# Performance work log

Measured on AMD Instinct MI355X. Metric: run time of the kernel, lower is better.

## Reference

```python
import jax, jax.numpy as jnp
import numpy as np

N = 50000       # nodes
E = 800000      # edges (avg degree 16)
D_IN = 128
D_H = 128
D_OUT = 64


def setup_inputs() -> dict:
    key = jax.random.key(0)
    ks = jax.random.split(key, 8)
    x = jax.random.normal(ks[0], (N, D_IN), dtype=jnp.float32)
    edge_index = jax.random.randint(ks[1], (2, E), 0, N)
    W1 = jax.random.normal(ks[2], (D_IN, D_H), dtype=jnp.float32) / np.sqrt(D_IN)
    b1 = jnp.zeros((D_H,), dtype=jnp.float32)
    W2 = jax.random.normal(ks[3], (D_H, D_H), dtype=jnp.float32) / np.sqrt(D_H)
    b2 = jnp.zeros((D_H,), dtype=jnp.float32)
    Wfc = jax.random.normal(ks[4], (D_H, D_OUT), dtype=jnp.float32) / np.sqrt(D_H)
    bfc = jnp.zeros((D_OUT,), dtype=jnp.float32)
    return {"x": x, "edge_index": edge_index, "W1": W1, "b1": b1,
            "W2": W2, "b2": b2, "Wfc": Wfc, "bfc": bfc}


def reference(x, edge_index, W1, b1, W2, b2, Wfc, bfc):
    n = x.shape[0]
    # GCNConv (PyG default): add self-loops, symmetric normalization
    loops = jnp.arange(n, dtype=edge_index.dtype)
    src = jnp.concatenate([edge_index[0], loops])
    dst = jnp.concatenate([edge_index[1], loops])
    deg = jax.ops.segment_sum(jnp.ones(src.shape, x.dtype), dst, num_segments=n)
    dinv = jnp.where(deg > 0, jax.lax.rsqrt(deg), jnp.zeros_like(deg))
    norm = dinv[src] * dinv[dst]  # [E + N]

    def gcn_conv(h, W, b):
        hw = h @ W                              # transform first (smaller gather)
        msg = hw[src] * norm[:, None]           # gather + scale
        return jax.ops.segment_sum(msg, dst, num_segments=n) + b  # scatter-add

    h = jax.nn.relu(gcn_conv(x, W1, b1))   # dropout_prob=0 -> identity
    h = jax.nn.relu(gcn_conv(h, W2, b2))
    pooled = jnp.max(h, axis=0)            # custom_global_max_pool over nodes
    return pooled @ Wfc + bfc              # [D_OUT]
```

## Files before the change

### kernel.cpp

```cpp
#include <hip/hip_runtime.h>
#include <cstdint>
#include <cstddef>

typedef unsigned int uint;
typedef unsigned short ushort;

__device__ __forceinline__ ushort f2bf(float f) {
    uint u = __float_as_uint(f);
    u = u + 0x7FFFu + ((u >> 16) & 1u);
    return (ushort)(u >> 16);
}
__device__ __forceinline__ float bf_lo(uint u) { return __uint_as_float((u & 0xFFFFu) << 16); }
__device__ __forceinline__ float bf_hi(uint u) { return __uint_as_float(u & 0xFFFF0000u); }


__global__ __launch_bounds__(256) void k_count(const int* __restrict__ dst,
                                               int* __restrict__ cnt,
                                               int* __restrict__ rank, int E) {
    int e4 = (blockIdx.x * 256 + threadIdx.x) * 4;
    if (e4 + 3 < E) {
        int4 d = *reinterpret_cast<const int4*>(&dst[e4]);
        int4 r;
        r.x = atomicAdd(&cnt[d.x], 1);
        r.y = atomicAdd(&cnt[d.y], 1);
        r.z = atomicAdd(&cnt[d.z], 1);
        r.w = atomicAdd(&cnt[d.w], 1);
        *reinterpret_cast<int4*>(&rank[e4]) = r;
    } else {
        for (int e = e4; e < E; e++)
            rank[e] = atomicAdd(&cnt[dst[e]], 1);
    }
}

__global__ __launch_bounds__(256) void k_block_reduce(const int* __restrict__ cnt,
                                                      int* __restrict__ bsum, int n) {
    __shared__ int sd[256];
    int i = blockIdx.x * 256 + threadIdx.x;
    sd[threadIdx.x] = (i < n) ? cnt[i] : 0;
    __syncthreads();
    for (int s = 128; s > 0; s >>= 1) {
        if (threadIdx.x < s) sd[threadIdx.x] += sd[threadIdx.x + s];
        __syncthreads();
    }
    if (threadIdx.x == 0) bsum[blockIdx.x] = sd[0];
}

__global__ __launch_bounds__(256) void k_scan_write(const int* __restrict__ cnt,
                                                    const int* __restrict__ bsum,
                                                    int* __restrict__ rowptr,
                                                    float* __restrict__ dinv,
                                                    int n, int nb) {
    __shared__ int sd[256];
    int t = threadIdx.x;
    sd[t] = (t < (int)blockIdx.x && t < nb) ? bsum[t] : 0;
    __syncthreads();
    for (int s = 128; s > 0; s >>= 1) {
        if (t < s) sd[t] += sd[t + s];
        __syncthreads();
    }
    int prefix = sd[0];
    __syncthreads();
    int i = blockIdx.x * 256 + t;
    int v = (i < n) ? cnt[i] : 0;
    sd[t] = v;
    __syncthreads();
    for (int off = 1; off < 256; off <<= 1) {
        int add = (t >= off) ? sd[t - off] : 0;
        __syncthreads();
        sd[t] += add;
        __syncthreads();
    }
    int excl = sd[t] - v + prefix;
    if (i < n) {
        rowptr[i] = excl;
        dinv[i] = rsqrtf((float)v + 1.0f);
    }
}

__global__ __launch_bounds__(256) void k_scatter(const int* __restrict__ src,
                                                 const int* __restrict__ dst,
                                                 const int* __restrict__ rowptr,
                                                 const int* __restrict__ rank,
                                                 const float* __restrict__ dinv,
                                                 int2* __restrict__ eSW, int E) {
    int e4 = (blockIdx.x * 256 + threadIdx.x) * 4;
    if (e4 + 3 < E) {
        int4 s = *reinterpret_cast<const int4*>(&src[e4]);
        int4 d = *reinterpret_cast<const int4*>(&dst[e4]);
        int4 r = *reinterpret_cast<const int4*>(&rank[e4]);
        int2 p0, p1, p2, p3;
        p0.x = s.x; p0.y = __float_as_int(dinv[s.x] * dinv[d.x]);
        p1.x = s.y; p1.y = __float_as_int(dinv[s.y] * dinv[d.y]);
        p2.x = s.z; p2.y = __float_as_int(dinv[s.z] * dinv[d.z]);
        p3.x = s.w; p3.y = __float_as_int(dinv[s.w] * dinv[d.w]);
        eSW[rowptr[d.x] + r.x] = p0;
        eSW[rowptr[d.y] + r.y] = p1;
        eSW[rowptr[d.z] + r.z] = p2;
        eSW[rowptr[d.w] + r.w] = p3;
    } else {
        for (int e = e4; e < E; e++) {
            int s = src[e], d = dst[e];
            int2 pp; pp.x = s; pp.y = __float_as_int(dinv[s] * dinv[d]);
            eSW[rowptr[d] + rank[e]] = pp;
        }
    }
}


#define AP 68

__global__ __launch_bounds__(256, 4) void k_gemm128(const float* __restrict__ A,
                                                    const float* __restrict__ Wg,
                                                    ushort* __restrict__ C, int nrows) {
    __shared__ float As[32 * AP];
    __shared__ float Ws[32 * 128];
    const int tid = threadIdx.x;
    const int tc = tid & 15;
    const int tr = tid >> 4;
    const int r0 = blockIdx.x * 64;

    float acc[4][8];
#pragma unroll
    for (int j = 0; j < 4; j++)
#pragma unroll
        for (int c = 0; c < 8; c++) acc[j][c] = 0.0f;

    const float4* A4 = reinterpret_cast<const float4*>(A);
    const float4* Wg4 = reinterpret_cast<const float4*>(Wg);
    float4* Ws4 = reinterpret_cast<float4*>(Ws);

    const int srow = tid >> 3;
    const int sk4 = tid & 7;

    for (int kc = 0; kc < 4; kc++) {
#pragma unroll
        for (int i = 0; i < 4; i++) Ws4[tid + 256 * i] = Wg4[kc * 1024 + tid + 256 * i];
#pragma unroll
        for (int pass = 0; pass < 2; pass++) {
            int rl = srow + pass * 32;
            int rg = r0 + rl;
            if (rg > nrows - 1) rg = nrows - 1;
            float4 av = A4[(size_t)rg * 32 + kc * 8 + sk4];
            int kb = sk4 * 4;
            As[(kb + 0) * AP + rl] = av.x;
            As[(kb + 1) * AP + rl] = av.y;
            As[(kb + 2) * AP + rl] = av.z;
            As[(kb + 3) * AP + rl] = av.w;
        }
        __syncthreads();

#pragma unroll 4
        for (int k = 0; k < 32; k++) {
            const float4 a = *reinterpret_cast<const float4*>(&As[k * AP + tr * 4]);
            const float4 w0 = *reinterpret_cast<const float4*>(&Ws[k * 128 + tc * 8]);
            const float4 w1 = *reinterpret_cast<const float4*>(&Ws[k * 128 + tc * 8 + 4]);
            const float av4[4] = {a.x, a.y, a.z, a.w};
            const float wv[8] = {w0.x, w0.y, w0.z, w0.w, w1.x, w1.y, w1.z, w1.w};
#pragma unroll
            for (int j = 0; j < 4; j++)
#pragma unroll
                for (int c = 0; c < 8; c++)
                    acc[j][c] = fmaf(av4[j], wv[c], acc[j][c]);
        }
        __syncthreads();
    }

#pragma unroll
    for (int j = 0; j < 4; j++) {
        const int r = r0 + tr * 4 + j;
        if (r < nrows) {
            uint4 o;
            o.x = (uint)f2bf(acc[j][0]) | ((uint)f2bf(acc[j][1]) << 16);
            o.y = (uint)f2bf(acc[j][2]) | ((uint)f2bf(acc[j][3]) << 16);
            o.z = (uint)f2bf(acc[j][4]) | ((uint)f2bf(acc[j][5]) << 16);
            o.w = (uint)f2bf(acc[j][6]) | ((uint)f2bf(acc[j][7]) << 16);
            *reinterpret_cast<uint4*>(&C[(size_t)r * 128 + tc * 8]) = o;
        }
    }
}


__global__ __launch_bounds__(256) void k_gather(const ushort* __restrict__ hw,
                                                const float* __restrict__ dinv,
                                                const int* __restrict__ rowptr,
                                                const int* __restrict__ cnt,
                                                const int2* __restrict__ eSW,
                                                const float* __restrict__ bias,
                                                float* __restrict__ outp, int n) {
    int wave = threadIdx.x >> 6;
    int lane = threadIdx.x & 63;
    int half = lane >> 5;
    int sub = lane & 31;
    int node = blockIdx.x * 4 + wave;
    if (node >= n) return;

    float di = dinv[node];
    int start = rowptr[node];
    int deg = cnt[node];

    const uint2* base2 = reinterpret_cast<const uint2*>(hw);
    float a0, a1, a2, a3;
    {
        uint2 u = base2[(size_t)node * 32 + sub];
        float sw = half ? 0.0f : di * di;
        a0 = bf_lo(u.x) * sw; a1 = bf_hi(u.x) * sw;
        a2 = bf_lo(u.y) * sw; a3 = bf_hi(u.y) * sw;
    }

    int j = 0;
    for (; j + 8 <= deg; j += 8) {
        int2 e[4]; uint2 u[4];
#pragma unroll
        for (int t = 0; t < 4; t++) e[t] = eSW[start + j + 2 * t + half];
#pragma unroll
        for (int t = 0; t < 4; t++) u[t] = base2[(size_t)e[t].x * 32 + sub];
#pragma unroll
        for (int t = 0; t < 4; t++) {
            float w = __int_as_float(e[t].y);
            a0 = fmaf(bf_lo(u[t].x), w, a0);
            a1 = fmaf(bf_hi(u[t].x), w, a1);
            a2 = fmaf(bf_lo(u[t].y), w, a2);
            a3 = fmaf(bf_hi(u[t].y), w, a3);
        }
    }
    for (; j < deg; j += 2) {
        int idx = j + half;
        bool ok = idx < deg;
        int2 e = eSW[start + (ok ? idx : deg - 1)];
        float w = ok ? __int_as_float(e.y) : 0.0f;
        uint2 u = base2[(size_t)e.x * 32 + sub];
        a0 = fmaf(bf_lo(u.x), w, a0);
        a1 = fmaf(bf_hi(u.x), w, a1);
        a2 = fmaf(bf_lo(u.y), w, a2);
        a3 = fmaf(bf_hi(u.y), w, a3);
    }

    a0 += __shfl_xor(a0, 32);
    a1 += __shfl_xor(a1, 32);
    a2 += __shfl_xor(a2, 32);
    a3 += __shfl_xor(a3, 32);

    if (half == 0) {
        float4 bb = reinterpret_cast<const float4*>(bias)[sub];
        float4 o;
        o.x = fmaxf(a0 + bb.x, 0.0f);
        o.y = fmaxf(a1 + bb.y, 0.0f);
        o.z = fmaxf(a2 + bb.z, 0.0f);
        o.w = fmaxf(a3 + bb.w, 0.0f);
        reinterpret_cast<float4*>(outp + (size_t)node * 128)[sub] = o;
    }
}


__global__ __launch_bounds__(256) void k_gather_pool(const ushort* __restrict__ hw,
                                                     const float* __restrict__ dinv,
                                                     const int* __restrict__ rowptr,
                                                     const int* __restrict__ cnt,
                                                     const int2* __restrict__ eSW,
                                                     const float* __restrict__ bias,
                                                     int* __restrict__ pooledPart, int n) {
    __shared__ int smax[128];
    int tid = threadIdx.x;
    int wave = tid >> 6;
    int lane = tid & 63;
    int half = lane >> 5;
    int sub = lane & 31;
    if (tid < 128) smax[tid] = 0;
    __syncthreads();

    int node = blockIdx.x * 4 + wave;
    if (node < n) {
        float di = dinv[node];
        int start = rowptr[node];
        int deg = cnt[node];

        const uint2* base2 = reinterpret_cast<const uint2*>(hw);
        float a0, a1, a2, a3;
        {
            uint2 u = base2[(size_t)node * 32 + sub];
            float sw = half ? 0.0f : di * di;
            a0 = bf_lo(u.x) * sw; a1 = bf_hi(u.x) * sw;
            a2 = bf_lo(u.y) * sw; a3 = bf_hi(u.y) * sw;
        }

        int j = 0;
        for (; j + 8 <= deg; j += 8) {
            int2 e[4]; uint2 u[4];
#pragma unroll
            for (int t = 0; t < 4; t++) e[t] = eSW[start + j + 2 * t + half];
#pragma unroll
            for (int t = 0; t < 4; t++) u[t] = base2[(size_t)e[t].x * 32 + sub];
#pragma unroll
            for (int t = 0; t < 4; t++) {
                float w = __int_as_float(e[t].y);
                a0 = fmaf(bf_lo(u[t].x), w, a0);
                a1 = fmaf(bf_hi(u[t].x), w, a1);
                a2 = fmaf(bf_lo(u[t].y), w, a2);
                a3 = fmaf(bf_hi(u[t].y), w, a3);
            }
        }
        for (; j < deg; j += 2) {
            int idx = j + half;
            bool ok = idx < deg;
            int2 e = eSW[start + (ok ? idx : deg - 1)];
            float w = ok ? __int_as_float(e.y) : 0.0f;
            uint2 u = base2[(size_t)e.x * 32 + sub];
            a0 = fmaf(bf_lo(u.x), w, a0);
            a1 = fmaf(bf_hi(u.x), w, a1);
            a2 = fmaf(bf_lo(u.y), w, a2);
            a3 = fmaf(bf_hi(u.y), w, a3);
        }

        a0 += __shfl_xor(a0, 32);
        a1 += __shfl_xor(a1, 32);
        a2 += __shfl_xor(a2, 32);
        a3 += __shfl_xor(a3, 32);

        if (half == 0) {
            float4 bb = reinterpret_cast<const float4*>(bias)[sub];
            a0 = fmaxf(a0 + bb.x, 0.0f);
            a1 = fmaxf(a1 + bb.y, 0.0f);
            a2 = fmaxf(a2 + bb.z, 0.0f);
            a3 = fmaxf(a3 + bb.w, 0.0f);
            atomicMax(&smax[sub * 4 + 0], __float_as_int(a0));
            atomicMax(&smax[sub * 4 + 1], __float_as_int(a1));
            atomicMax(&smax[sub * 4 + 2], __float_as_int(a2));
            atomicMax(&smax[sub * 4 + 3], __float_as_int(a3));
        }
    }
    __syncthreads();
    if (tid < 128) pooledPart[(size_t)blockIdx.x * 128 + tid] = smax[tid];
}


__global__ __launch_bounds__(256) void k_pool2fc(const int* __restrict__ pooledPart,
                                                 int* __restrict__ pooledBits,
                                                 int* __restrict__ ticket,
                                                 const float* __restrict__ Wfc,
                                                 const float* __restrict__ bfc,
                                                 float* __restrict__ out, int nPart) {
    __shared__ int smax[128];
    __shared__ int isLast;
    int tid = threadIdx.x;
    int c = tid & 127;
    int rh = tid >> 7;
    if (tid < 128) smax[tid] = 0;
    __syncthreads();
    int m = 0;
    for (int p = blockIdx.x * 2 + rh; p < nPart; p += gridDim.x * 2) {
        int v = pooledPart[(size_t)p * 128 + c];
        m = v > m ? v : m;
    }
    atomicMax(&smax[c], m);
    __syncthreads();
    if (tid < 128) atomicMax(&pooledBits[tid], smax[tid]);
    __threadfence();
    if (tid == 0) isLast = (atomicAdd(ticket, 1) == (int)gridDim.x - 1) ? 1 : 0;
    __syncthreads();
    if (isLast) {
        __threadfence();
        if (tid < 128) smax[tid] = atomicMax(&pooledBits[tid], 0);
        __syncthreads();
        if (tid < 64) {
            float acc = bfc[tid];
            for (int k = 0; k < 128; k++)
                acc = fmaf(__int_as_float(smax[k]), Wfc[k * 64 + tid], acc);
            out[tid] = acc;
        }
    }
}


extern "C" void kernel_launch(void* const* d_in, const int* in_sizes, int n_in,
                              void* d_out, int out_size, void* d_ws, size_t ws_size,
                              hipStream_t stream) {
    const float* x   = (const float*)d_in[0];
    const int* edges = (const int*)d_in[1];
    const float* W1  = (const float*)d_in[2];
    const float* b1  = (const float*)d_in[3];
    const float* W2  = (const float*)d_in[4];
    const float* b2  = (const float*)d_in[5];
    const float* Wfc = (const float*)d_in[6];
    const float* bfc = (const float*)d_in[7];
    float* out = (float*)d_out;

    const int N = in_sizes[0] / 128;
    const int E = in_sizes[1] / 2;
    const int* esrc_in = edges;
    const int* edst_in = edges + E;

    auto align256 = [](size_t v) { return (v + 255) & ~(size_t)255; };
    char* p = (char*)d_ws;
    size_t off = 0;
    int* cnt      = (int*)(p + off); off += (size_t)N * 4;
    int* ticket   = (int*)(p + off); off = align256(off + 4);
    int* rowptr   = (int*)(p + off); off = align256(off + (size_t)N * 4);
    int* rank     = (int*)(p + off); off = align256(off + (size_t)E * 4);
    float* dinv   = (float*)(p + off); off = align256(off + (size_t)N * 4);
    int* bsum     = (int*)(p + off); off = align256(off + 256 * 4);
    int* pooled   = (int*)(p + off); off = align256(off + 128 * 4);
    int2* eSW     = (int2*)(p + off); off = align256(off + (size_t)E * 8);
    ushort* hwbuf = (ushort*)(p + off); off = align256(off + (size_t)N * 128 * 2);
    float* hbuf   = (float*)(p + off); off = align256(off + (size_t)N * 128 * 4);
    (void)ws_size; (void)n_in; (void)out_size;

    const int EB4 = (E / 4 + 255) / 256;
    const int NB = (N + 255) / 256;
    const int GB = (N + 63) / 64;
    const int HB = (N + 3) / 4;

    int* pooledPart = (int*)hbuf;

    hipMemsetAsync(cnt, 0, (size_t)N * 4 + 4, stream);

    k_count<<<EB4, 256, 0, stream>>>(edst_in, cnt, rank, E);
    k_block_reduce<<<NB, 256, 0, stream>>>(cnt, bsum, N);
    k_scan_write<<<NB, 256, 0, stream>>>(cnt, bsum, rowptr, dinv, N, NB);
    k_scatter<<<EB4, 256, 0, stream>>>(esrc_in, edst_in, rowptr, rank, dinv, eSW, E);

    k_gemm128<<<GB, 256, 0, stream>>>(x, W1, hwbuf, N);
    k_gather<<<HB, 256, 0, stream>>>(hwbuf, dinv, rowptr, cnt, eSW, b1, hbuf, N);
    k_gemm128<<<GB, 256, 0, stream>>>(hbuf, W2, hwbuf, N);
    k_gather_pool<<<HB, 256, 0, stream>>>(hwbuf, dinv, rowptr, cnt, eSW, b2, pooledPart, N);

    k_pool2fc<<<128, 256, 0, stream>>>(pooledPart, pooled, ticket, Wfc, bfc, out, HB);
}
```

Baseline: 309.2 us.

## Pack edge source and source degree into 32 bits; recompute norm in gather

```diff
diff --git a/kernel.cpp b/kernel.cpp
--- a/kernel.cpp
+++ b/kernel.cpp
@@ -17,17 +17,23 @@
 __global__ __launch_bounds__(256) void k_count(const int* __restrict__ dst,
                                                int* __restrict__ cnt,
                                                int* __restrict__ rank, int E) {
-    int e4 = (blockIdx.x * 256 + threadIdx.x) * 4;
-    if (e4 + 3 < E) {
-        int4 d = *reinterpret_cast<const int4*>(&dst[e4]);
-        int4 r;
-        r.x = atomicAdd(&cnt[d.x], 1);
-        r.y = atomicAdd(&cnt[d.y], 1);
-        r.z = atomicAdd(&cnt[d.z], 1);
-        r.w = atomicAdd(&cnt[d.w], 1);
-        *reinterpret_cast<int4*>(&rank[e4]) = r;
+    int e8 = (blockIdx.x * 256 + threadIdx.x) * 8;
+    if (e8 + 7 < E) {
+        int4 d0 = *reinterpret_cast<const int4*>(&dst[e8]);
+        int4 d1 = *reinterpret_cast<const int4*>(&dst[e8 + 4]);
+        int4 r0, r1;
+        r0.x = atomicAdd(&cnt[d0.x], 1);
+        r0.y = atomicAdd(&cnt[d0.y], 1);
+        r0.z = atomicAdd(&cnt[d0.z], 1);
+        r0.w = atomicAdd(&cnt[d0.w], 1);
+        r1.x = atomicAdd(&cnt[d1.x], 1);
+        r1.y = atomicAdd(&cnt[d1.y], 1);
+        r1.z = atomicAdd(&cnt[d1.z], 1);
+        r1.w = atomicAdd(&cnt[d1.w], 1);
+        *reinterpret_cast<int4*>(&rank[e8]) = r0;
+        *reinterpret_cast<int4*>(&rank[e8 + 4]) = r1;
     } else {
-        for (int e = e4; e < E; e++)
+        for (int e = e8; e < E; e++)
             rank[e] = atomicAdd(&cnt[dst[e]], 1);
     }
 }
@@ -48,7 +54,6 @@
 __global__ __launch_bounds__(256) void k_scan_write(const int* __restrict__ cnt,
                                                     const int* __restrict__ bsum,
                                                     int* __restrict__ rowptr,
-                                                    float* __restrict__ dinv,
                                                     int n, int nb) {
     __shared__ int sd[256];
     int t = threadIdx.x;
@@ -70,38 +75,28 @@
         sd[t] += add;
         __syncthreads();
     }
-    int excl = sd[t] - v + prefix;
-    if (i < n) {
-        rowptr[i] = excl;
-        dinv[i] = rsqrtf((float)v + 1.0f);
-    }
+    if (i < n) rowptr[i] = sd[t] - v + prefix;
 }
 
 __global__ __launch_bounds__(256) void k_scatter(const int* __restrict__ src,
                                                  const int* __restrict__ dst,
                                                  const int* __restrict__ rowptr,
                                                  const int* __restrict__ rank,
-                                                 const float* __restrict__ dinv,
-                                                 int2* __restrict__ eSW, int E) {
+                                                 const int* __restrict__ cnt,
+                                                 uint* __restrict__ eSW, int E) {
     int e4 = (blockIdx.x * 256 + threadIdx.x) * 4;
     if (e4 + 3 < E) {
         int4 s = *reinterpret_cast<const int4*>(&src[e4]);
         int4 d = *reinterpret_cast<const int4*>(&dst[e4]);
         int4 r = *reinterpret_cast<const int4*>(&rank[e4]);
-        int2 p0, p1, p2, p3;
-        p0.x = s.x; p0.y = __float_as_int(dinv[s.x] * dinv[d.x]);
-        p1.x = s.y; p1.y = __float_as_int(dinv[s.y] * dinv[d.y]);
-        p2.x = s.z; p2.y = __float_as_int(dinv[s.z] * dinv[d.z]);
-        p3.x = s.w; p3.y = __float_as_int(dinv[s.w] * dinv[d.w]);
-        eSW[rowptr[d.x] + r.x] = p0;
-        eSW[rowptr[d.y] + r.y] = p1;
-        eSW[rowptr[d.z] + r.z] = p2;
-        eSW[rowptr[d.w] + r.w] = p3;
+        eSW[rowptr[d.x] + r.x] = (uint)s.x | ((uint)cnt[s.x] << 16);
+        eSW[rowptr[d.y] + r.y] = (uint)s.y | ((uint)cnt[s.y] << 16);
+        eSW[rowptr[d.z] + r.z] = (uint)s.z | ((uint)cnt[s.z] << 16);
+        eSW[rowptr[d.w] + r.w] = (uint)s.w | ((uint)cnt[s.w] << 16);
     } else {
         for (int e = e4; e < E; e++) {
             int s = src[e], d = dst[e];
-            int2 pp; pp.x = s; pp.y = __float_as_int(dinv[s] * dinv[d]);
-            eSW[rowptr[d] + rank[e]] = pp;
+            eSW[rowptr[d] + rank[e]] = (uint)s | ((uint)cnt[s] << 16);
         }
     }
 }
@@ -181,10 +176,9 @@
 
 
 __global__ __launch_bounds__(256) void k_gather(const ushort* __restrict__ hw,
-                                                const float* __restrict__ dinv,
                                                 const int* __restrict__ rowptr,
                                                 const int* __restrict__ cnt,
-                                                const int2* __restrict__ eSW,
+                                                const uint* __restrict__ eSW,
                                                 const float* __restrict__ bias,
                                                 float* __restrict__ outp, int n) {
     int wave = threadIdx.x >> 6;
@@ -194,9 +188,10 @@
     int node = blockIdx.x * 4 + wave;
     if (node >= n) return;
 
-    float di = dinv[node];
     int start = rowptr[node];
     int deg = cnt[node];
+    float dd1 = (float)(deg + 1);
+    float di = rsqrtf(dd1);
 
     const uint2* base2 = reinterpret_cast<const uint2*>(hw);
     float a0, a1, a2, a3;
@@ -209,14 +204,14 @@
 
     int j = 0;
     for (; j + 8 <= deg; j += 8) {
-        int2 e[4]; uint2 u[4];
+        uint e[4]; uint2 u[4];
 #pragma unroll
         for (int t = 0; t < 4; t++) e[t] = eSW[start + j + 2 * t + half];
 #pragma unroll
-        for (int t = 0; t < 4; t++) u[t] = base2[(size_t)e[t].x * 32 + sub];
+        for (int t = 0; t < 4; t++) u[t] = base2[(size_t)(e[t] & 0xFFFFu) * 32 + sub];
 #pragma unroll
         for (int t = 0; t < 4; t++) {
-            float w = __int_as_float(e[t].y);
+            float w = rsqrtf((float)((e[t] >> 16) + 1u) * dd1);
             a0 = fmaf(bf_lo(u[t].x), w, a0);
             a1 = fmaf(bf_hi(u[t].x), w, a1);
             a2 = fmaf(bf_lo(u[t].y), w, a2);
@@ -226,9 +221,9 @@
     for (; j < deg; j += 2) {
         int idx = j + half;
         bool ok = idx < deg;
-        int2 e = eSW[start + (ok ? idx : deg - 1)];
-        float w = ok ? __int_as_float(e.y) : 0.0f;
-        uint2 u = base2[(size_t)e.x * 32 + sub];
+        uint e = eSW[start + (ok ? idx : deg - 1)];
+        float w = ok ? rsqrtf((float)((e >> 16) + 1u) * dd1) : 0.0f;
+        uint2 u = base2[(size_t)(e & 0xFFFFu) * 32 + sub];
         a0 = fmaf(bf_lo(u.x), w, a0);
         a1 = fmaf(bf_hi(u.x), w, a1);
         a2 = fmaf(bf_lo(u.y), w, a2);
@@ -253,10 +248,9 @@
 
 
 __global__ __launch_bounds__(256) void k_gather_pool(const ushort* __restrict__ hw,
-                                                     const float* __restrict__ dinv,
                                                      const int* __restrict__ rowptr,
                                                      const int* __restrict__ cnt,
-                                                     const int2* __restrict__ eSW,
+                                                     const uint* __restrict__ eSW,
                                                      const float* __restrict__ bias,
                                                      int* __restrict__ pooledPart, int n) {
     __shared__ int smax[128];
@@ -270,9 +264,10 @@
 
     int node = blockIdx.x * 4 + wave;
     if (node < n) {
-        float di = dinv[node];
         int start = rowptr[node];
         int deg = cnt[node];
+        float dd1 = (float)(deg + 1);
+        float di = rsqrtf(dd1);
 
         const uint2* base2 = reinterpret_cast<const uint2*>(hw);
         float a0, a1, a2, a3;
@@ -285,14 +280,14 @@
 
         int j = 0;
         for (; j + 8 <= deg; j += 8) {
-            int2 e[4]; uint2 u[4];
+            uint e[4]; uint2 u[4];
 #pragma unroll
             for (int t = 0; t < 4; t++) e[t] = eSW[start + j + 2 * t + half];
 #pragma unroll
-            for (int t = 0; t < 4; t++) u[t] = base2[(size_t)e[t].x * 32 + sub];
+            for (int t = 0; t < 4; t++) u[t] = base2[(size_t)(e[t] & 0xFFFFu) * 32 + sub];
 #pragma unroll
             for (int t = 0; t < 4; t++) {
-                float w = __int_as_float(e[t].y);
+                float w = rsqrtf((float)((e[t] >> 16) + 1u) * dd1);
                 a0 = fmaf(bf_lo(u[t].x), w, a0);
                 a1 = fmaf(bf_hi(u[t].x), w, a1);
                 a2 = fmaf(bf_lo(u[t].y), w, a2);
@@ -302,9 +297,9 @@
         for (; j < deg; j += 2) {
             int idx = j + half;
             bool ok = idx < deg;
-            int2 e = eSW[start + (ok ? idx : deg - 1)];
-            float w = ok ? __int_as_float(e.y) : 0.0f;
-            uint2 u = base2[(size_t)e.x * 32 + sub];
+            uint e = eSW[start + (ok ? idx : deg - 1)];
+            float w = ok ? rsqrtf((float)((e >> 16) + 1u) * dd1) : 0.0f;
+            uint2 u = base2[(size_t)(e & 0xFFFFu) * 32 + sub];
             a0 = fmaf(bf_lo(u.x), w, a0);
             a1 = fmaf(bf_hi(u.x), w, a1);
             a2 = fmaf(bf_lo(u.y), w, a2);
@@ -396,14 +391,14 @@
     int* ticket   = (int*)(p + off); off = align256(off + 4);
     int* rowptr   = (int*)(p + off); off = align256(off + (size_t)N * 4);
     int* rank     = (int*)(p + off); off = align256(off + (size_t)E * 4);
-    float* dinv   = (float*)(p + off); off = align256(off + (size_t)N * 4);
     int* bsum     = (int*)(p + off); off = align256(off + 256 * 4);
     int* pooled   = (int*)(p + off); off = align256(off + 128 * 4);
-    int2* eSW     = (int2*)(p + off); off = align256(off + (size_t)E * 8);
+    uint* eSW     = (uint*)(p + off); off = align256(off + (size_t)E * 4);
     ushort* hwbuf = (ushort*)(p + off); off = align256(off + (size_t)N * 128 * 2);
     float* hbuf   = (float*)(p + off); off = align256(off + (size_t)N * 128 * 4);
     (void)ws_size; (void)n_in; (void)out_size;
 
+    const int EB8 = (E / 8 + 255) / 256;
     const int EB4 = (E / 4 + 255) / 256;
     const int NB = (N + 255) / 256;
     const int GB = (N + 63) / 64;
@@ -413,15 +408,15 @@
 
     hipMemsetAsync(cnt, 0, (size_t)N * 4 + 4, stream);
 
-    k_count<<<EB4, 256, 0, stream>>>(edst_in, cnt, rank, E);
+    k_count<<<EB8, 256, 0, stream>>>(edst_in, cnt, rank, E);
     k_block_reduce<<<NB, 256, 0, stream>>>(cnt, bsum, N);
-    k_scan_write<<<NB, 256, 0, stream>>>(cnt, bsum, rowptr, dinv, N, NB);
-    k_scatter<<<EB4, 256, 0, stream>>>(esrc_in, edst_in, rowptr, rank, dinv, eSW, E);
+    k_scan_write<<<NB, 256, 0, stream>>>(cnt, bsum, rowptr, N, NB);
+    k_scatter<<<EB4, 256, 0, stream>>>(esrc_in, edst_in, rowptr, rank, cnt, eSW, E);
 
     k_gemm128<<<GB, 256, 0, stream>>>(x, W1, hwbuf, N);
-    k_gather<<<HB, 256, 0, stream>>>(hwbuf, dinv, rowptr, cnt, eSW, b1, hbuf, N);
+    k_gather<<<HB, 256, 0, stream>>>(hwbuf, rowptr, cnt, eSW, b1, hbuf, N);
     k_gemm128<<<GB, 256, 0, stream>>>(hbuf, W2, hwbuf, N);
-    k_gather_pool<<<HB, 256, 0, stream>>>(hwbuf, dinv, rowptr, cnt, eSW, b2, pooledPart, N);
+    k_gather_pool<<<HB, 256, 0, stream>>>(hwbuf, rowptr, cnt, eSW, b2, pooledPart, N);
 
     k_pool2fc<<<128, 256, 0, stream>>>(pooledPart, pooled, ticket, Wfc, bfc, out, HB);
 }
```

After: 298.8 us. 3.4% less time.
